# Optimization experiments

Hardware: AMD Instinct MI355X
Metric: run time of the kernel (lower is better)

Reference implementation:

```python
import jax, jax.numpy as jnp
import numpy as np

LN_EPS = 1e-5
K = 6
NUM_KP = 5


def decoder_res_cat(x, w1, b1, gamma, beta, w2, b2):
    # MLP = relu(LayerNorm(Linear(x))); out = Linear(cat([x, MLP(x)]))
    h = x @ w1 + b1
    mu = h.mean(axis=-1, keepdims=True)
    var = ((h - mu) ** 2).mean(axis=-1, keepdims=True)
    h = jax.nn.relu(gamma * (h - mu) / jnp.sqrt(var + LN_EPS) + beta)
    return jnp.concatenate([x, h], axis=-1) @ w2 + b2


def setup_inputs() -> dict:
    key = jax.random.key(0)
    ks = jax.random.split(key, 8)
    B, S, E, H = 2048, 134, 256, 1024
    s = 0.02
    return {
        "hidden_output": jax.random.normal(ks[0], (B, S, E), jnp.float32),
        "future_key_points": jax.random.normal(ks[1], (B, NUM_KP, 2), jnp.float32),
        "ld_w1": jax.random.normal(ks[2], (E, H), jnp.float32) * s,
        "ld_b1": jnp.zeros((H,), jnp.float32),
        "ld_gamma": jnp.ones((H,), jnp.float32),
        "ld_beta": jnp.zeros((H,), jnp.float32),
        "ld_w2": jax.random.normal(ks[3], (E + H, 2 * K), jnp.float32) * s,
        "ld_b2": jnp.zeros((2 * K,), jnp.float32),
        "sd_w1": jax.random.normal(ks[4], (E, H), jnp.float32) * s,
        "sd_b1": jnp.zeros((H,), jnp.float32),
        "sd_gamma": jnp.ones((H,), jnp.float32),
        "sd_beta": jnp.zeros((H,), jnp.float32),
        "sd_w2": jax.random.normal(ks[5], (E + H, K), jnp.float32) * s,
        "sd_b2": jnp.zeros((K,), jnp.float32),
        "context_length": 128,
    }


def reference(hidden_output, future_key_points, ld_w1, ld_b1, ld_gamma, ld_beta,
              ld_w2, ld_b2, sd_w1, sd_b1, sd_gamma, sd_beta, sd_w2, sd_b2,
              context_length):
    B, T = future_key_points.shape[0], future_key_points.shape[1]
    kp_start = context_length - 1  # use_proposal=False
    h = jax.lax.dynamic_slice_in_dim(hidden_output, kp_start, T, axis=1)  # [B,T,E]

    logits = decoder_res_cat(h, ld_w1, ld_b1, ld_gamma, ld_beta, ld_w2, ld_b2)
    logits = logits.reshape(B, T, K, 2)                                   # [B,T,K,2]
    scores = decoder_res_cat(h, sd_w1, sd_b1, sd_gamma, sd_beta, sd_w2, sd_b2)  # [B,T,K]

    # per-mode MSE(reduction='none') summed over xy -> [B,T,K]
    sq = (logits - future_key_points[:, :, None, :2]) ** 2
    loss_bk = sq.sum(axis=-1)
    min_loss = loss_bk.min(axis=-1)           # [B,T]
    min_idx = loss_bk.argmin(axis=-1)         # [B,T] int

    # CrossEntropyLoss applied to softmax(scores) (faithful double-softmax)
    sm = jax.nn.softmax(scores, axis=-1)
    logp = jax.nn.log_softmax(sm, axis=-1)
    ce = -jnp.take_along_axis(logp, min_idx[..., None], axis=-1)[..., 0]  # [B,T]

    weights = 0.1 ** (4.0 - jnp.arange(T, dtype=jnp.float32))             # [T]
    loss_per_kp = min_loss.mean(axis=0) * weights + ce.mean(axis=0)       # [T]

    selected = jnp.take_along_axis(logits, min_idx[:, :, None, None], axis=2)[:, :, 0, :]  # [B,T,2]
    kp_loss = loss_per_kp.mean() * 1.0  # kp_loss_rescale=1.0
    return kp_loss, logits, scores, selected, loss_per_kp
```

## Files before the change

### kernel.cpp

```cpp
#include <hip/hip_runtime.h>
#include <math.h>

#define B_    2048
#define S_    134
#define E_    256
#define H_    1024
#define T_    5
#define KK_   6
#define NROWS (B_*T_)
#define R_    8
#define NBLK  (NROWS/R_)

#define OFF_LOGITS 1
#define OFF_SCORES (OFF_LOGITS + NROWS*12)
#define OFF_SEL    (OFF_SCORES + NROWS*6)
#define OFF_LPK    (OFF_SEL + NROWS*2)

template<int NOUT>
__device__ __forceinline__ void decoder_phase(
    const float (*xs)[E_],
    const float* __restrict__ w1, const float* __restrict__ b1,
    const float* __restrict__ ga, const float* __restrict__ be,
    const float* __restrict__ w2, const float* __restrict__ b2,
    float (*hs)[H_], float (*red)[4][2], float* mu_s, float* rs_s,
    float* osh, float* __restrict__ gout, int g0, int tid)
{
    const int wave = tid >> 6;
    const int lane = tid & 63;
    const int j0   = tid * 4;

    float acc[R_][4];
#pragma unroll
    for (int r = 0; r < R_; ++r) {
        acc[r][0] = 0.f; acc[r][1] = 0.f; acc[r][2] = 0.f; acc[r][3] = 0.f;
    }

    for (int k0 = 0; k0 < E_; k0 += 8) {
        float4 w[8];
#pragma unroll
        for (int kk = 0; kk < 8; ++kk)
            w[kk] = *(const float4*)(w1 + (size_t)(k0 + kk)*H_ + j0);
#pragma unroll
        for (int r = 0; r < R_; ++r) {
            float4 xa = *(const float4*)&xs[r][k0];
            float4 xb = *(const float4*)&xs[r][k0+4];
            acc[r][0] += xa.x*w[0].x; acc[r][1] += xa.x*w[0].y; acc[r][2] += xa.x*w[0].z; acc[r][3] += xa.x*w[0].w;
            acc[r][0] += xa.y*w[1].x; acc[r][1] += xa.y*w[1].y; acc[r][2] += xa.y*w[1].z; acc[r][3] += xa.y*w[1].w;
            acc[r][0] += xa.z*w[2].x; acc[r][1] += xa.z*w[2].y; acc[r][2] += xa.z*w[2].z; acc[r][3] += xa.z*w[2].w;
            acc[r][0] += xa.w*w[3].x; acc[r][1] += xa.w*w[3].y; acc[r][2] += xa.w*w[3].z; acc[r][3] += xa.w*w[3].w;
            acc[r][0] += xb.x*w[4].x; acc[r][1] += xb.x*w[4].y; acc[r][2] += xb.x*w[4].z; acc[r][3] += xb.x*w[4].w;
            acc[r][0] += xb.y*w[5].x; acc[r][1] += xb.y*w[5].y; acc[r][2] += xb.y*w[5].z; acc[r][3] += xb.y*w[5].w;
            acc[r][0] += xb.z*w[6].x; acc[r][1] += xb.z*w[6].y; acc[r][2] += xb.z*w[6].z; acc[r][3] += xb.z*w[6].w;
            acc[r][0] += xb.w*w[7].x; acc[r][1] += xb.w*w[7].y; acc[r][2] += xb.w*w[7].z; acc[r][3] += xb.w*w[7].w;
        }
    }

    {
        float4 bv = *(const float4*)(b1 + j0);
#pragma unroll
        for (int r = 0; r < R_; ++r) {
            acc[r][0] += bv.x; acc[r][1] += bv.y; acc[r][2] += bv.z; acc[r][3] += bv.w;
        }
    }

#pragma unroll
    for (int r = 0; r < R_; ++r) {
        float s  = acc[r][0] + acc[r][1] + acc[r][2] + acc[r][3];
        float ss = acc[r][0]*acc[r][0] + acc[r][1]*acc[r][1]
                 + acc[r][2]*acc[r][2] + acc[r][3]*acc[r][3];
#pragma unroll
        for (int off = 32; off > 0; off >>= 1) {
            s  += __shfl_xor(s,  off, 64);
            ss += __shfl_xor(ss, off, 64);
        }
        if (lane == 0) { red[r][wave][0] = s; red[r][wave][1] = ss; }
    }
    __syncthreads();
    if (tid < R_) {
        float s  = red[tid][0][0] + red[tid][1][0] + red[tid][2][0] + red[tid][3][0];
        float ss = red[tid][0][1] + red[tid][1][1] + red[tid][2][1] + red[tid][3][1];
        float mu  = s * (1.0f / H_);
        float var = ss * (1.0f / H_) - mu * mu;
        mu_s[tid] = mu;
        rs_s[tid] = rsqrtf(var + 1e-5f);
    }
    __syncthreads();

    {
        float4 gv = *(const float4*)(ga + j0);
        float4 bv = *(const float4*)(be + j0);
#pragma unroll
        for (int r = 0; r < R_; ++r) {
            float mu = mu_s[r], rs = rs_s[r];
            float4 hv;
            hv.x = gv.x * ((acc[r][0] - mu) * rs) + bv.x;
            hv.y = gv.y * ((acc[r][1] - mu) * rs) + bv.y;
            hv.z = gv.z * ((acc[r][2] - mu) * rs) + bv.z;
            hv.w = gv.w * ((acc[r][3] - mu) * rs) + bv.w;
            hv.x = hv.x > 0.f ? hv.x : 0.f;
            hv.y = hv.y > 0.f ? hv.y : 0.f;
            hv.z = hv.z > 0.f ? hv.z : 0.f;
            hv.w = hv.w > 0.f ? hv.w : 0.f;
            *(float4*)&hs[r][j0] = hv;
        }
    }
    __syncthreads();

    float p[2][NOUT];
#pragma unroll
    for (int rr = 0; rr < 2; ++rr)
#pragma unroll
        for (int n = 0; n < NOUT; ++n) p[rr][n] = 0.f;

    const int jbase = lane * 20;
#pragma unroll
    for (int jj = 0; jj < 20; ++jj) {
        const int j = jbase + jj;
        float w2r[NOUT];
#pragma unroll
        for (int n = 0; n < NOUT; ++n) w2r[n] = w2[(size_t)j*NOUT + n];
#pragma unroll
        for (int rr = 0; rr < 2; ++rr) {
            const int r = wave*2 + rr;
            float v = (j < E_) ? xs[r][j] : hs[r][j - E_];
#pragma unroll
            for (int n = 0; n < NOUT; ++n) p[rr][n] += v * w2r[n];
        }
    }
#pragma unroll
    for (int rr = 0; rr < 2; ++rr)
#pragma unroll
        for (int n = 0; n < NOUT; ++n)
#pragma unroll
            for (int off = 32; off > 0; off >>= 1)
                p[rr][n] += __shfl_xor(p[rr][n], off, 64);

    if (lane == 0) {
#pragma unroll
        for (int rr = 0; rr < 2; ++rr) {
            const int r = wave*2 + rr;
            const int g = g0 + r;
#pragma unroll
            for (int n = 0; n < NOUT; ++n) {
                float v = p[rr][n] + b2[n];
                osh[r*NOUT + n] = v;
                gout[(size_t)g*NOUT + n] = v;
            }
        }
    }
    __syncthreads();
}

__global__ __launch_bounds__(256, 3)
void kp_fused(const float* __restrict__ hid,  const float* __restrict__ fkp,
              const float* __restrict__ w1ld, const float* __restrict__ b1ld,
              const float* __restrict__ gld,  const float* __restrict__ btld,
              const float* __restrict__ w2ld, const float* __restrict__ b2ld,
              const float* __restrict__ w1sd, const float* __restrict__ b1sd,
              const float* __restrict__ gsd,  const float* __restrict__ btsd,
              const float* __restrict__ w2sd, const float* __restrict__ b2sd,
              const int* __restrict__ ctx,
              float* __restrict__ out, float* __restrict__ ws)
{
    __shared__ float hs[R_][H_];
    __shared__ float xs[R_][E_];
    __shared__ float red[R_][4][2];
    __shared__ float mu_s[R_], rs_s[R_];
    __shared__ float lo_s[R_*12];
    __shared__ float sc_s[R_*6];

    const int tid = threadIdx.x;
    const int g0  = blockIdx.x * R_;
    const int kp0 = ctx[0] - 1;

    {
        const int r   = tid >> 5;
        const int off = (tid & 31) * 8;
        const int g = g0 + r;
        const int b = g / T_;
        const int t = g - b * T_;
        const float* src = hid + (size_t)(b * S_ + kp0 + t) * E_ + off;
        float4 v0 = *(const float4*)(src);
        float4 v1 = *(const float4*)(src + 4);
        *(float4*)&xs[r][off]     = v0;
        *(float4*)&xs[r][off + 4] = v1;
    }
    __syncthreads();

    decoder_phase<12>(xs, w1ld, b1ld, gld, btld, w2ld, b2ld,
                      hs, red, mu_s, rs_s, lo_s, out + OFF_LOGITS, g0, tid);
    decoder_phase<6>(xs, w1sd, b1sd, gsd, btsd, w2sd, b2sd,
                     hs, red, mu_s, rs_s, sc_s, out + OFF_SCORES, g0, tid);

    if (tid < R_) {
        const int g = g0 + tid;
        const int b = g / T_;
        const int t = g - b * T_;
        const float y0 = fkp[b*(T_*2) + t*2 + 0];
        const float y1 = fkp[b*(T_*2) + t*2 + 1];

        float best = 1e30f; int am = 0;
#pragma unroll
        for (int k = 0; k < KK_; ++k) {
            float dx = lo_s[tid*12 + 2*k + 0] - y0;
            float dy = lo_s[tid*12 + 2*k + 1] - y1;
            float L = dx*dx + dy*dy;
            if (L < best) { best = L; am = k; }
        }

        float m = -1e30f;
#pragma unroll
        for (int k = 0; k < KK_; ++k) m = fmaxf(m, sc_s[tid*6 + k]);
        float e[KK_]; float ssum = 0.f;
#pragma unroll
        for (int k = 0; k < KK_; ++k) { e[k] = expf(sc_s[tid*6 + k] - m); ssum += e[k]; }
        const float inv = 1.0f / ssum;
        float lse = 0.f, sm_am = 0.f;
#pragma unroll
        for (int k = 0; k < KK_; ++k) {
            float smk = e[k] * inv;
            lse += expf(smk);
            if (k == am) sm_am = smk;
        }
        const float ce = logf(lse) - sm_am;

        out[OFF_SEL + g*2 + 0] = lo_s[tid*12 + 2*am + 0];
        out[OFF_SEL + g*2 + 1] = lo_s[tid*12 + 2*am + 1];

        atomicAdd(&ws[t],       best);
        atomicAdd(&ws[T_ + t],  ce);
    }
}

__global__ void kp_finalize(const float* __restrict__ ws, float* __restrict__ out)
{
    if (threadIdx.x == 0 && blockIdx.x == 0) {
        const float wts[T_] = {1e-4f, 1e-3f, 1e-2f, 1e-1f, 1.0f};
        float s = 0.f;
#pragma unroll
        for (int t = 0; t < T_; ++t) {
            float ml = ws[t]      * (1.0f / B_);
            float ce = ws[T_ + t] * (1.0f / B_);
            float l  = ml * wts[t] + ce;
            out[OFF_LPK + t] = l;
            s += l;
        }
        out[0] = s * (1.0f / T_);
    }
}

extern "C" void kernel_launch(void* const* d_in, const int* in_sizes, int n_in,
                              void* d_out, int out_size, void* d_ws, size_t ws_size,
                              hipStream_t stream)
{
    const float* hid  = (const float*)d_in[0];
    const float* fkp  = (const float*)d_in[1];
    const float* w1ld = (const float*)d_in[2];
    const float* b1ld = (const float*)d_in[3];
    const float* gld  = (const float*)d_in[4];
    const float* btld = (const float*)d_in[5];
    const float* w2ld = (const float*)d_in[6];
    const float* b2ld = (const float*)d_in[7];
    const float* w1sd = (const float*)d_in[8];
    const float* b1sd = (const float*)d_in[9];
    const float* gsd  = (const float*)d_in[10];
    const float* btsd = (const float*)d_in[11];
    const float* w2sd = (const float*)d_in[12];
    const float* b2sd = (const float*)d_in[13];
    const int*   ctx  = (const int*)d_in[14];
    float* out = (float*)d_out;
    float* ws  = (float*)d_ws;

    hipMemsetAsync(ws, 0, 2 * T_ * sizeof(float), stream);

    kp_fused<<<NBLK, 256, 0, stream>>>(hid, fkp,
                                       w1ld, b1ld, gld, btld, w2ld, b2ld,
                                       w1sd, b1sd, gsd, btsd, w2sd, b2sd,
                                       ctx, out, ws);
    kp_finalize<<<1, 64, 0, stream>>>(ws, out);
}
```

Measured before the change: 532.7 us.

## Double rows per block, stream x from global, software-pipeline W1 loads

Raises rows per block from 8 to 16 so each W1 column load is reused across twice as many rows. The shared-memory x staging is dropped: x is read directly from global/L1 inside the GEMM loop. W1 loads are double-buffered in two halves, and the second GEMM is split into two 8-row halves so the hs buffer stays the size it was before. Launch bounds go to 4 blocks per CU. The cost is 64 accumulator registers per thread, which risks spills or lower occupancy, plus uncoalesced broadcast global reads of x in the inner loop.

```diff
diff --git a/kernel.cpp b/kernel.cpp
--- a/kernel.cpp
+++ b/kernel.cpp
@@ -8,7 +8,7 @@
 #define T_    5
 #define KK_   6
 #define NROWS (B_*T_)
-#define R_    8
+#define R_    16
 #define NBLK  (NROWS/R_)
 
 #define OFF_LOGITS 1
@@ -17,8 +17,72 @@
 #define OFF_LPK    (OFF_SEL + NROWS*2)
 
 template<int NOUT>
+__device__ __forceinline__ void gemm2_half(
+    const float* __restrict__ hid, int kp0, int g0, int rowbase,
+    const float (*hs)[H_],
+    const float* __restrict__ w2, const float* __restrict__ b2,
+    float* osh, float* __restrict__ gout, int tid)
+{
+    const int wave = tid >> 6;
+    const int lane = tid & 63;
+
+    float p[2][NOUT];
+#pragma unroll
+    for (int rr = 0; rr < 2; ++rr)
+#pragma unroll
+        for (int n = 0; n < NOUT; ++n) p[rr][n] = 0.f;
+
+    const float* xptr[2];
+#pragma unroll
+    for (int rr = 0; rr < 2; ++rr) {
+        const int lr = wave*2 + rr;
+        const int g  = g0 + rowbase + lr;
+        const int b  = g / T_;
+        const int t  = g - b * T_;
+        xptr[rr] = hid + (size_t)(b * S_ + kp0 + t) * E_;
+    }
+
+    const int jbase = lane * 20;
+#pragma unroll
+    for (int jj = 0; jj < 20; ++jj) {
+        const int j = jbase + jj;
+        float w2r[NOUT];
+#pragma unroll
+        for (int n = 0; n < NOUT; ++n) w2r[n] = w2[(size_t)j*NOUT + n];
+#pragma unroll
+        for (int rr = 0; rr < 2; ++rr) {
+            const int lr = wave*2 + rr;
+            float v = (j < E_) ? xptr[rr][j] : hs[lr][j - E_];
+#pragma unroll
+            for (int n = 0; n < NOUT; ++n) p[rr][n] += v * w2r[n];
+        }
+    }
+#pragma unroll
+    for (int rr = 0; rr < 2; ++rr)
+#pragma unroll
+        for (int n = 0; n < NOUT; ++n)
+#pragma unroll
+            for (int off = 32; off > 0; off >>= 1)
+                p[rr][n] += __shfl_xor(p[rr][n], off, 64);
+
+    if (lane == 0) {
+#pragma unroll
+        for (int rr = 0; rr < 2; ++rr) {
+            const int lr = wave*2 + rr;
+            const int g  = g0 + rowbase + lr;
+#pragma unroll
+            for (int n = 0; n < NOUT; ++n) {
+                float v = p[rr][n] + b2[n];
+                osh[(rowbase + lr)*NOUT + n] = v;
+                gout[(size_t)g*NOUT + n] = v;
+            }
+        }
+    }
+}
+
+template<int NOUT>
 __device__ __forceinline__ void decoder_phase(
-    const float (*xs)[E_],
+    const float* __restrict__ hid, int kp0,
     const float* __restrict__ w1, const float* __restrict__ b1,
     const float* __restrict__ ga, const float* __restrict__ be,
     const float* __restrict__ w2, const float* __restrict__ b2,
@@ -29,29 +93,51 @@
     const int lane = tid & 63;
     const int j0   = tid * 4;
 
+    size_t xoff[R_];
+#pragma unroll
+    for (int r = 0; r < R_; ++r) {
+        const int g = g0 + r;
+        const int b = g / T_;
+        const int t = g - b * T_;
+        xoff[r] = (size_t)(b * S_ + kp0 + t) * E_;
+    }
+
     float acc[R_][4];
 #pragma unroll
     for (int r = 0; r < R_; ++r) {
         acc[r][0] = 0.f; acc[r][1] = 0.f; acc[r][2] = 0.f; acc[r][3] = 0.f;
     }
 
+    const float* wcol = w1 + j0;
+    float4 wa[4], wb[4];
+#pragma unroll
+    for (int kk = 0; kk < 4; ++kk)
+        wa[kk] = *(const float4*)(wcol + (size_t)kk*H_);
+
     for (int k0 = 0; k0 < E_; k0 += 8) {
-        float4 w[8];
-#pragma unroll
-        for (int kk = 0; kk < 8; ++kk)
-            w[kk] = *(const float4*)(w1 + (size_t)(k0 + kk)*H_ + j0);
+#pragma unroll
+        for (int kk = 0; kk < 4; ++kk)
+            wb[kk] = *(const float4*)(wcol + (size_t)(k0+4+kk)*H_);
 #pragma unroll
         for (int r = 0; r < R_; ++r) {
-            float4 xa = *(const float4*)&xs[r][k0];
-            float4 xb = *(const float4*)&xs[r][k0+4];
-            acc[r][0] += xa.x*w[0].x; acc[r][1] += xa.x*w[0].y; acc[r][2] += xa.x*w[0].z; acc[r][3] += xa.x*w[0].w;
-            acc[r][0] += xa.y*w[1].x; acc[r][1] += xa.y*w[1].y; acc[r][2] += xa.y*w[1].z; acc[r][3] += xa.y*w[1].w;
-            acc[r][0] += xa.z*w[2].x; acc[r][1] += xa.z*w[2].y; acc[r][2] += xa.z*w[2].z; acc[r][3] += xa.z*w[2].w;
-            acc[r][0] += xa.w*w[3].x; acc[r][1] += xa.w*w[3].y; acc[r][2] += xa.w*w[3].z; acc[r][3] += xa.w*w[3].w;
-            acc[r][0] += xb.x*w[4].x; acc[r][1] += xb.x*w[4].y; acc[r][2] += xb.x*w[4].z; acc[r][3] += xb.x*w[4].w;
-            acc[r][0] += xb.y*w[5].x; acc[r][1] += xb.y*w[5].y; acc[r][2] += xb.y*w[5].z; acc[r][3] += xb.y*w[5].w;
-            acc[r][0] += xb.z*w[6].x; acc[r][1] += xb.z*w[6].y; acc[r][2] += xb.z*w[6].z; acc[r][3] += xb.z*w[6].w;
-            acc[r][0] += xb.w*w[7].x; acc[r][1] += xb.w*w[7].y; acc[r][2] += xb.w*w[7].z; acc[r][3] += xb.w*w[7].w;
+            float4 xv = *(const float4*)(hid + xoff[r] + k0);
+            acc[r][0] += xv.x*wa[0].x; acc[r][1] += xv.x*wa[0].y; acc[r][2] += xv.x*wa[0].z; acc[r][3] += xv.x*wa[0].w;
+            acc[r][0] += xv.y*wa[1].x; acc[r][1] += xv.y*wa[1].y; acc[r][2] += xv.y*wa[1].z; acc[r][3] += xv.y*wa[1].w;
+            acc[r][0] += xv.z*wa[2].x; acc[r][1] += xv.z*wa[2].y; acc[r][2] += xv.z*wa[2].z; acc[r][3] += xv.z*wa[2].w;
+            acc[r][0] += xv.w*wa[3].x; acc[r][1] += xv.w*wa[3].y; acc[r][2] += xv.w*wa[3].z; acc[r][3] += xv.w*wa[3].w;
+        }
+        if (k0 + 8 < E_) {
+#pragma unroll
+            for (int kk = 0; kk < 4; ++kk)
+                wa[kk] = *(const float4*)(wcol + (size_t)(k0+8+kk)*H_);
+        }
+#pragma unroll
+        for (int r = 0; r < R_; ++r) {
+            float4 xv = *(const float4*)(hid + xoff[r] + k0 + 4);
+            acc[r][0] += xv.x*wb[0].x; acc[r][1] += xv.x*wb[0].y; acc[r][2] += xv.x*wb[0].z; acc[r][3] += xv.x*wb[0].w;
+            acc[r][0] += xv.y*wb[1].x; acc[r][1] += xv.y*wb[1].y; acc[r][2] += xv.y*wb[1].z; acc[r][3] += xv.y*wb[1].w;
+            acc[r][0] += xv.z*wb[2].x; acc[r][1] += xv.z*wb[2].y; acc[r][2] += xv.z*wb[2].z; acc[r][3] += xv.z*wb[2].w;
+            acc[r][0] += xv.w*wb[3].x; acc[r][1] += xv.w*wb[3].y; acc[r][2] += xv.w*wb[3].z; acc[r][3] += xv.w*wb[3].w;
         }
     }
 
@@ -92,66 +178,32 @@
 #pragma unroll
         for (int r = 0; r < R_; ++r) {
             float mu = mu_s[r], rs = rs_s[r];
-            float4 hv;
-            hv.x = gv.x * ((acc[r][0] - mu) * rs) + bv.x;
-            hv.y = gv.y * ((acc[r][1] - mu) * rs) + bv.y;
-            hv.z = gv.z * ((acc[r][2] - mu) * rs) + bv.z;
-            hv.w = gv.w * ((acc[r][3] - mu) * rs) + bv.w;
-            hv.x = hv.x > 0.f ? hv.x : 0.f;
-            hv.y = hv.y > 0.f ? hv.y : 0.f;
-            hv.z = hv.z > 0.f ? hv.z : 0.f;
-            hv.w = hv.w > 0.f ? hv.w : 0.f;
-            *(float4*)&hs[r][j0] = hv;
-        }
-    }
-    __syncthreads();
-
-    float p[2][NOUT];
-#pragma unroll
-    for (int rr = 0; rr < 2; ++rr)
-#pragma unroll
-        for (int n = 0; n < NOUT; ++n) p[rr][n] = 0.f;
-
-    const int jbase = lane * 20;
-#pragma unroll
-    for (int jj = 0; jj < 20; ++jj) {
-        const int j = jbase + jj;
-        float w2r[NOUT];
-#pragma unroll
-        for (int n = 0; n < NOUT; ++n) w2r[n] = w2[(size_t)j*NOUT + n];
-#pragma unroll
-        for (int rr = 0; rr < 2; ++rr) {
-            const int r = wave*2 + rr;
-            float v = (j < E_) ? xs[r][j] : hs[r][j - E_];
-#pragma unroll
-            for (int n = 0; n < NOUT; ++n) p[rr][n] += v * w2r[n];
-        }
-    }
-#pragma unroll
-    for (int rr = 0; rr < 2; ++rr)
-#pragma unroll
-        for (int n = 0; n < NOUT; ++n)
-#pragma unroll
-            for (int off = 32; off > 0; off >>= 1)
-                p[rr][n] += __shfl_xor(p[rr][n], off, 64);
-
-    if (lane == 0) {
-#pragma unroll
-        for (int rr = 0; rr < 2; ++rr) {
-            const int r = wave*2 + rr;
-            const int g = g0 + r;
-#pragma unroll
-            for (int n = 0; n < NOUT; ++n) {
-                float v = p[rr][n] + b2[n];
-                osh[r*NOUT + n] = v;
-                gout[(size_t)g*NOUT + n] = v;
-            }
-        }
-    }
-    __syncthreads();
-}
-
-__global__ __launch_bounds__(256, 3)
+            float h0 = gv.x * ((acc[r][0] - mu) * rs) + bv.x;
+            float h1 = gv.y * ((acc[r][1] - mu) * rs) + bv.y;
+            float h2 = gv.z * ((acc[r][2] - mu) * rs) + bv.z;
+            float h3 = gv.w * ((acc[r][3] - mu) * rs) + bv.w;
+            acc[r][0] = h0 > 0.f ? h0 : 0.f;
+            acc[r][1] = h1 > 0.f ? h1 : 0.f;
+            acc[r][2] = h2 > 0.f ? h2 : 0.f;
+            acc[r][3] = h3 > 0.f ? h3 : 0.f;
+        }
+    }
+
+#pragma unroll
+    for (int r = 0; r < 8; ++r)
+        *(float4*)&hs[r][j0] = *(float4*)&acc[r][0];
+    __syncthreads();
+    gemm2_half<NOUT>(hid, kp0, g0, 0, hs, w2, b2, osh, gout, tid);
+    __syncthreads();
+#pragma unroll
+    for (int r = 0; r < 8; ++r)
+        *(float4*)&hs[r][j0] = *(float4*)&acc[8 + r][0];
+    __syncthreads();
+    gemm2_half<NOUT>(hid, kp0, g0, 8, hs, w2, b2, osh, gout, tid);
+    __syncthreads();
+}
+
+__global__ __launch_bounds__(256, 4)
 void kp_fused(const float* __restrict__ hid,  const float* __restrict__ fkp,
               const float* __restrict__ w1ld, const float* __restrict__ b1ld,
               const float* __restrict__ gld,  const float* __restrict__ btld,
@@ -162,8 +214,7 @@
               const int* __restrict__ ctx,
               float* __restrict__ out, float* __restrict__ ws)
 {
-    __shared__ float hs[R_][H_];
-    __shared__ float xs[R_][E_];
+    __shared__ float hs[8][H_];
     __shared__ float red[R_][4][2];
     __shared__ float mu_s[R_], rs_s[R_];
     __shared__ float lo_s[R_*12];
@@ -173,23 +224,9 @@
     const int g0  = blockIdx.x * R_;
     const int kp0 = ctx[0] - 1;
 
-    {
-        const int r   = tid >> 5;
-        const int off = (tid & 31) * 8;
-        const int g = g0 + r;
-        const int b = g / T_;
-        const int t = g - b * T_;
-        const float* src = hid + (size_t)(b * S_ + kp0 + t) * E_ + off;
-        float4 v0 = *(const float4*)(src);
-        float4 v1 = *(const float4*)(src + 4);
-        *(float4*)&xs[r][off]     = v0;
-        *(float4*)&xs[r][off + 4] = v1;
-    }
-    __syncthreads();
-
-    decoder_phase<12>(xs, w1ld, b1ld, gld, btld, w2ld, b2ld,
+    decoder_phase<12>(hid, kp0, w1ld, b1ld, gld, btld, w2ld, b2ld,
                       hs, red, mu_s, rs_s, lo_s, out + OFF_LOGITS, g0, tid);
-    decoder_phase<6>(xs, w1sd, b1sd, gsd, btsd, w2sd, b2sd,
+    decoder_phase<6>(hid, kp0, w1sd, b1sd, gsd, btsd, w2sd, b2sd,
                      hs, red, mu_s, rs_s, sc_s, out + OFF_SCORES, g0, tid);
 
     if (tid < R_) {
```

Result: slower. 694.4 us (+30.4%).

## Process sixteen rows per block, running the output projection in two halves

Applied to the files above, without the earlier changes.

Doubles the rows handled per block from 8 to 16, so each W1 element loaded from memory is reused across twice as many rows in the first GEMM. To keep shared memory bounded, the hidden activations stay in registers and are staged into an 8-row shared buffer twice, with the second projection split into two half passes. Launch bounds drop to two blocks per SM to make room for the larger register accumulator. The costs are more registers per thread, lower occupancy, fewer blocks in flight, and extra barriers.

```diff
diff --git a/kernel.cpp b/kernel.cpp
--- a/kernel.cpp
+++ b/kernel.cpp
@@ -8,13 +8,67 @@
 #define T_    5
 #define KK_   6
 #define NROWS (B_*T_)
-#define R_    8
+#define R_    16
 #define NBLK  (NROWS/R_)
 
 #define OFF_LOGITS 1
 #define OFF_SCORES (OFF_LOGITS + NROWS*12)
 #define OFF_SEL    (OFF_SCORES + NROWS*6)
 #define OFF_LPK    (OFF_SEL + NROWS*2)
+
+template<int NOUT>
+__device__ __forceinline__ void gemm2_half(
+    const float (*xs)[E_], int g0, int rowbase,
+    const float (*hs)[H_],
+    const float* __restrict__ w2, const float* __restrict__ b2,
+    float* osh, float* __restrict__ gout, int tid)
+{
+    const int wave = tid >> 6;
+    const int lane = tid & 63;
+
+    float p[2][NOUT];
+#pragma unroll
+    for (int rr = 0; rr < 2; ++rr)
+#pragma unroll
+        for (int n = 0; n < NOUT; ++n) p[rr][n] = 0.f;
+
+    const int jbase = lane * 20;
+#pragma unroll
+    for (int jj = 0; jj < 20; ++jj) {
+        const int j = jbase + jj;
+        float w2r[NOUT];
+#pragma unroll
+        for (int n = 0; n < NOUT; ++n) w2r[n] = w2[(size_t)j*NOUT + n];
+#pragma unroll
+        for (int rr = 0; rr < 2; ++rr) {
+            const int lr = wave*2 + rr;
+            float v = (j < E_) ? xs[rowbase + lr][j] : hs[lr][j - E_];
+#pragma unroll
+            for (int n = 0; n < NOUT; ++n) p[rr][n] += v * w2r[n];
+        }
+    }
+#pragma unroll
+    for (int rr = 0; rr < 2; ++rr)
+#pragma unroll
+        for (int n = 0; n < NOUT; ++n)
+#pragma unroll
+            for (int off = 32; off > 0; off >>= 1)
+                p[rr][n] += __shfl_xor(p[rr][n], off, 64);
+
+    if (lane == 0) {
+#pragma unroll
+        for (int rr = 0; rr < 2; ++rr) {
+            const int lr = wave*2 + rr;
+            const int g  = g0 + rowbase + lr;
+#pragma unroll
+            for (int n = 0; n < NOUT; ++n) {
+                float v = p[rr][n] + b2[n];
+                osh[(rowbase + lr)*NOUT + n] = v;
+                gout[(size_t)g*NOUT + n] = v;
+            }
+        }
+    }
+}
 
 template<int NOUT>
 __device__ __forceinline__ void decoder_phase(
@@ -92,66 +146,32 @@
 #pragma unroll
         for (int r = 0; r < R_; ++r) {
             float mu = mu_s[r], rs = rs_s[r];
-            float4 hv;
-            hv.x = gv.x * ((acc[r][0] - mu) * rs) + bv.x;
-            hv.y = gv.y * ((acc[r][1] - mu) * rs) + bv.y;
-            hv.z = gv.z * ((acc[r][2] - mu) * rs) + bv.z;
-            hv.w = gv.w * ((acc[r][3] - mu) * rs) + bv.w;
-            hv.x = hv.x > 0.f ? hv.x : 0.f;
-            hv.y = hv.y > 0.f ? hv.y : 0.f;
-            hv.z = hv.z > 0.f ? hv.z : 0.f;
-            hv.w = hv.w > 0.f ? hv.w : 0.f;
-            *(float4*)&hs[r][j0] = hv;
-        }
-    }
-    __syncthreads();
-
-    float p[2][NOUT];
-#pragma unroll
-    for (int rr = 0; rr < 2; ++rr)
-#pragma unroll
-        for (int n = 0; n < NOUT; ++n) p[rr][n] = 0.f;
-
-    const int jbase = lane * 20;
-#pragma unroll
-    for (int jj = 0; jj < 20; ++jj) {
-        const int j = jbase + jj;
-        float w2r[NOUT];
-#pragma unroll
-        for (int n = 0; n < NOUT; ++n) w2r[n] = w2[(size_t)j*NOUT + n];
-#pragma unroll
-        for (int rr = 0; rr < 2; ++rr) {
-            const int r = wave*2 + rr;
-            float v = (j < E_) ? xs[r][j] : hs[r][j - E_];
-#pragma unroll
-            for (int n = 0; n < NOUT; ++n) p[rr][n] += v * w2r[n];
-        }
-    }
-#pragma unroll
-    for (int rr = 0; rr < 2; ++rr)
-#pragma unroll
-        for (int n = 0; n < NOUT; ++n)
-#pragma unroll
-            for (int off = 32; off > 0; off >>= 1)
-                p[rr][n] += __shfl_xor(p[rr][n], off, 64);
-
-    if (lane == 0) {
-#pragma unroll
-        for (int rr = 0; rr < 2; ++rr) {
-            const int r = wave*2 + rr;
-            const int g = g0 + r;
-#pragma unroll
-            for (int n = 0; n < NOUT; ++n) {
-                float v = p[rr][n] + b2[n];
-                osh[r*NOUT + n] = v;
-                gout[(size_t)g*NOUT + n] = v;
-            }
-        }
-    }
-    __syncthreads();
-}
-
-__global__ __launch_bounds__(256, 3)
+            float h0 = gv.x * ((acc[r][0] - mu) * rs) + bv.x;
+            float h1 = gv.y * ((acc[r][1] - mu) * rs) + bv.y;
+            float h2 = gv.z * ((acc[r][2] - mu) * rs) + bv.z;
+            float h3 = gv.w * ((acc[r][3] - mu) * rs) + bv.w;
+            acc[r][0] = h0 > 0.f ? h0 : 0.f;
+            acc[r][1] = h1 > 0.f ? h1 : 0.f;
+            acc[r][2] = h2 > 0.f ? h2 : 0.f;
+            acc[r][3] = h3 > 0.f ? h3 : 0.f;
+        }
+    }
+
+#pragma unroll
+    for (int r = 0; r < 8; ++r)
+        *(float4*)&hs[r][j0] = *(float4*)&acc[r][0];
+    __syncthreads();
+    gemm2_half<NOUT>(xs, g0, 0, hs, w2, b2, osh, gout, tid);
+    __syncthreads();
+#pragma unroll
+    for (int r = 0; r < 8; ++r)
+        *(float4*)&hs[r][j0] = *(float4*)&acc[8 + r][0];
+    __syncthreads();
+    gemm2_half<NOUT>(xs, g0, 8, hs, w2, b2, osh, gout, tid);
+    __syncthreads();
+}
+
+__global__ __launch_bounds__(256, 2)
 void kp_fused(const float* __restrict__ hid,  const float* __restrict__ fkp,
               const float* __restrict__ w1ld, const float* __restrict__ b1ld,
               const float* __restrict__ gld,  const float* __restrict__ btld,
@@ -162,7 +182,7 @@
               const int* __restrict__ ctx,
               float* __restrict__ out, float* __restrict__ ws)
 {
-    __shared__ float hs[R_][H_];
+    __shared__ float hs[8][H_];
     __shared__ float xs[R_][E_];
     __shared__ float red[R_][4][2];
     __shared__ float mu_s[R_], rs_s[R_];
@@ -174,16 +194,15 @@
     const int kp0 = ctx[0] - 1;
 
     {
-        const int r   = tid >> 5;
-        const int off = (tid & 31) * 8;
+        const int r   = tid >> 4;
+        const int off = (tid & 15) * 16;
         const int g = g0 + r;
         const int b = g / T_;
         const int t = g - b * T_;
         const float* src = hid + (size_t)(b * S_ + kp0 + t) * E_ + off;
-        float4 v0 = *(const float4*)(src);
-        float4 v1 = *(const float4*)(src + 4);
-        *(float4*)&xs[r][off]     = v0;
-        *(float4*)&xs[r][off + 4] = v1;
+#pragma unroll
+        for (int q = 0; q < 4; ++q)
+            *(float4*)&xs[r][off + 4*q] = *(const float4*)(src + 4*q);
     }
     __syncthreads();
 
```

New measurement: 750.4 us. 40.9% more time.
